# Optimization experiments

Hardware: AMD Instinct MI355X
Metric: run time of the kernel (lower is better)

The kernel has to match this reference:

```python
import jax, jax.numpy as jnp
import numpy as np

HID = 3584   # hidden_size
NH = 28      # num_attention_heads
NKV = 4      # num_key_value_heads
HD = 128     # head_dim
S = 4        # packed samples
L = 1024     # tokens per sample (sample_lens = [L]*S)
T = S * L
THETA = 1000000.0
EPS = 1e-6


def rmsnorm(x, w):
    # Qwen2NavitRMSNorm (fp32 math)
    v = jnp.mean(x * x, axis=-1, keepdims=True)
    return w * (x * jax.lax.rsqrt(v + EPS))


def rotate_half(x):
    d = x.shape[-1] // 2
    return jnp.concatenate([-x[..., d:], x[..., :d]], axis=-1)


def setup_inputs() -> dict:
    key = jax.random.key(0)
    ks = jax.random.split(key, 12)
    sc = 0.02
    x = jax.random.normal(ks[0], (T, HID), jnp.float32)
    # rotary embeddings: positions restart per packed sample
    pos = jnp.tile(jnp.arange(L, dtype=jnp.float32), S)
    inv = 1.0 / (THETA ** (jnp.arange(0, HD, 2, dtype=jnp.float32) / HD))
    fr = pos[:, None] * inv[None, :]
    emb = jnp.concatenate([fr, fr], axis=-1)  # [T, HD]
    und_idx = jnp.arange(0, T, 2, dtype=jnp.int32)  # interleaved und/gen tokens
    gen_idx = jnp.arange(1, T, 2, dtype=jnp.int32)
    n = lambda k, shp: jax.random.normal(k, shp, jnp.float32) * sc
    return dict(
        packed_sequence=x, cos=jnp.cos(emb), sin=jnp.sin(emb),
        wq=n(ks[1], (NH * HD, HID)), bq=jnp.zeros((NH * HD,), jnp.float32),
        wk=n(ks[2], (NKV * HD, HID)), bk=jnp.zeros((NKV * HD,), jnp.float32),
        wv=n(ks[3], (NKV * HD, HID)), bv=jnp.zeros((NKV * HD,), jnp.float32),
        wo=n(ks[4], (HID, NH * HD)),
        wqg=n(ks[5], (NH * HD, HID)), bqg=jnp.zeros((NH * HD,), jnp.float32),
        wkg=n(ks[6], (NKV * HD, HID)), bkg=jnp.zeros((NKV * HD,), jnp.float32),
        wvg=n(ks[7], (NKV * HD, HID)), bvg=jnp.zeros((NKV * HD,), jnp.float32),
        wog=n(ks[8], (HID, NH * HD)),
        qn=jnp.ones((HD,), jnp.float32), kn=jnp.ones((HD,), jnp.float32),
        qng=jnp.ones((HD,), jnp.float32), kng=jnp.ones((HD,), jnp.float32),
        und_idx=und_idx, gen_idx=gen_idx,
    )


def reference(packed_sequence, cos, sin, wq, bq, wk, bk, wv, bv, wo,
              wqg, bqg, wkg, bkg, wvg, bvg, wog, qn, kn, qng, kng,
              und_idx, gen_idx):
    x = packed_sequence
    xu = x[und_idx]
    xg = x[gen_idx]

    def dual_proj(wu, bu, wg, bg, dim):
        out = jnp.zeros((T, dim), x.dtype)
        out = out.at[und_idx].set(xu @ wu.T + bu)
        out = out.at[gen_idx].set(xg @ wg.T + bg)
        return out

    q = dual_proj(wq, bq, wqg, bqg, NH * HD).reshape(T, NH, HD)
    k = dual_proj(wk, bk, wkg, bkg, NKV * HD).reshape(T, NKV, HD)
    v = dual_proj(wv, bv, wvg, bvg, NKV * HD).reshape(T, NKV, HD)

    # per-modality qk RMSNorm
    q = jnp.zeros_like(q).at[und_idx].set(rmsnorm(q[und_idx], qn)).at[gen_idx].set(rmsnorm(q[gen_idx], qng))
    k = jnp.zeros_like(k).at[und_idx].set(rmsnorm(k[und_idx], kn)).at[gen_idx].set(rmsnorm(k[gen_idx], kng))

    # RoPE (unsqueeze_dim=1 -> broadcast over heads)
    c = cos[:, None, :]
    s = sin[:, None, :]
    q = q * c + rotate_half(q) * s
    k = k * c + rotate_half(k) * s

    # GQA expand kv heads (consecutive repeat matches repeat+reshape in torch)
    grp = NH // NKV
    k = jnp.repeat(k, grp, axis=1)  # [T, NH, HD]
    v = jnp.repeat(v, grp, axis=1)

    # packed -> per-sample causal attention (all sample_lens equal)
    qh = q.reshape(S, L, NH, HD)
    kh = k.reshape(S, L, NH, HD)
    vh = v.reshape(S, L, NH, HD)
    scores = jnp.einsum('slhd,smhd->shlm', qh, kh) / np.float32(np.sqrt(HD))
    causal = jnp.tril(jnp.ones((L, L), bool))
    scores = jnp.where(causal, scores, jnp.float32(-1e30))
    p = jax.nn.softmax(scores, axis=-1)
    attn = jnp.einsum('shlm,smhd->slhd', p, vh).reshape(T, NH * HD)

    out = jnp.zeros((T, HID), x.dtype)
    out = out.at[und_idx].set(attn[und_idx] @ wo.T)
    out = out.at[gen_idx].set(attn[gen_idx] @ wog.T)
    return out
```

## Files before the change

### kernel.cpp

```cpp
#include <hip/hip_runtime.h>
#include <hip/hip_bf16.h>

#define T_TOK 4096
#define HID   3584
#define NH    28
#define NKV   4
#define HD    128
#define SEG   4
#define LSEQ  1024
#define KDIM  3584
#define BKG   64
#define NCVT  128

typedef __attribute__((ext_vector_type(8))) short bf16x8;
typedef __attribute__((ext_vector_type(4))) float f32x4;

#define GLOAD16(g, l) __builtin_amdgcn_global_load_lds( \
    (const __attribute__((address_space(1))) void*)(g), \
    (__attribute__((address_space(3))) void*)(l), 16, 0, 0)

__device__ __forceinline__ unsigned short f2bf(float f) {
    unsigned u = __float_as_uint(f);
    return (unsigned short)((u + 0x7fffu + ((u >> 16) & 1u)) >> 16);
}
__device__ __forceinline__ float bf2f(unsigned short u) {
    return __uint_as_float(((unsigned)u) << 16);
}

__device__ __forceinline__ f32x4 mfma16(bf16x8 a, bf16x8 b, f32x4 c) {
    return __builtin_amdgcn_mfma_f32_16x16x32_bf16(a, b, c, 0, 0, 0);
}


__global__ void cvt4_f32_bf16(const float* __restrict__ s0, const float* __restrict__ s1,
                              const float* __restrict__ s2, const float* __restrict__ s3,
                              unsigned short* __restrict__ d0, unsigned short* __restrict__ d1,
                              unsigned short* __restrict__ d2, unsigned short* __restrict__ d3,
                              int n4) {
    const float* s; unsigned short* d;
    switch (blockIdx.y) {
        case 0: s = s0; d = d0; break;
        case 1: s = s1; d = d1; break;
        case 2: s = s2; d = d2; break;
        default: s = s3; d = d3; break;
    }
    int i = blockIdx.x * 256 + threadIdx.x;
    if (i >= n4) return;
    float4 v = reinterpret_cast<const float4*>(s)[i];
    ushort4 o;
    o.x = f2bf(v.x); o.y = f2bf(v.y); o.z = f2bf(v.z); o.w = f2bf(v.w);
    reinterpret_cast<ushort4*>(d)[i] = o;
}

__global__ void cvt_x_split(const float* __restrict__ x,
                            unsigned short* __restrict__ xu, unsigned short* __restrict__ xg) {
    int i = blockIdx.x * 256 + threadIdx.x;
    int t = i / (HID / 4);
    int c = i - t * (HID / 4);
    float4 v = reinterpret_cast<const float4*>(x)[i];
    ushort4 o;
    o.x = f2bf(v.x); o.y = f2bf(v.y); o.z = f2bf(v.z); o.w = f2bf(v.w);
    unsigned short* dst = ((t & 1) ? xg : xu) + (size_t)(t >> 1) * HID + c * 4;
    *reinterpret_cast<ushort4*>(dst) = o;
}

__device__ __forceinline__ void gemm256_core(const unsigned short* __restrict__ Aptr,
                                             const unsigned short* __restrict__ Bptr,
                                             unsigned short* ldsbase, f32x4 (&acc)[8][4],
                                             int kb, int kend) {
    const int tid = threadIdx.x;
    const int lane = tid & 63, w = tid >> 6;
    const int wr = w >> 2, wc = w & 3;
    const int lr = lane & 15, lkg = lane >> 4;
    char* const L = (char*)ldsbase;

    int src_off[4];
#pragma unroll
    for (int j = 0; j < 4; j++) {
        int r = j * 64 + (tid >> 3);
        int clog = (tid & 7) ^ ((tid >> 3) & 7);
        src_off[j] = r * KDIM + clog * 8;
    }
    const int aoff0 = (wr * 128 + lr) * 128 + ((lkg ^ (lr & 7)) << 4);
    const int boff0 = (wc * 64 + lr) * 128 + ((lkg ^ (lr & 7)) << 4) + 32768;

    bf16x8 a[4][2], b[4][2];
#pragma unroll
    for (int m = 0; m < 8; m++)
#pragma unroll
        for (int n = 0; n < 4; n++) acc[m][n] = (f32x4){0.f, 0.f, 0.f, 0.f};

#define STG_A(buf, k0, h) do { _Pragma("unroll") for (int jj = 0; jj < 2; jj++) { \
    int j = (h) * 2 + jj; \
    GLOAD16(Aptr + src_off[j] + (k0), L + (buf) * 65536 + j * 8192 + tid * 16); } } while (0)
#define STG_B(buf, k0, h) do { _Pragma("unroll") for (int jj = 0; jj < 2; jj++) { \
    int j = (h) * 2 + jj; \
    GLOAD16(Bptr + src_off[j] + (k0), L + (buf) * 65536 + 32768 + j * 8192 + tid * 16); } } while (0)
#define RD_A(buf, mh) do { _Pragma("unroll") for (int mm = 0; mm < 4; mm++) { \
    int ro = (buf) * 65536 + aoff0 + ((mh) * 4 + mm) * 2048; \
    a[mm][0] = *(const bf16x8*)(L + ro); \
    a[mm][1] = *(const bf16x8*)(L + (ro ^ 64)); } } while (0)
#define RD_B(buf, nh) do { _Pragma("unroll") for (int nn = 0; nn < 2; nn++) { \
    int ro = (buf) * 65536 + boff0 + ((nh) * 2 + nn) * 2048; \
    b[(nh) * 2 + nn][0] = *(const bf16x8*)(L + ro); \
    b[(nh) * 2 + nn][1] = *(const bf16x8*)(L + (ro ^ 64)); } } while (0)
#define MM(mh, nh) do { _Pragma("unroll") for (int mm = 0; mm < 4; mm++) \
    _Pragma("unroll") for (int nn = 0; nn < 2; nn++) \
    _Pragma("unroll") for (int ks = 0; ks < 2; ks++) \
        acc[(mh) * 4 + mm][(nh) * 2 + nn] = \
            mfma16(a[mm][ks], b[(nh) * 2 + nn][ks], acc[(mh) * 4 + mm][(nh) * 2 + nn]); } while (0)
#define BAR   asm volatile("s_barrier" ::: "memory")
#define LGKM0 do { asm volatile("s_waitcnt lgkmcnt(0)" ::: "memory"); \
                   __builtin_amdgcn_sched_barrier(0); } while (0)
#define VMC4  asm volatile("s_waitcnt vmcnt(4)" ::: "memory")
#define PHI   __builtin_amdgcn_s_setprio(1)
#define PLO   __builtin_amdgcn_s_setprio(0)

    STG_A(0, kb, 0); STG_A(0, kb, 1); STG_B(0, kb, 0); STG_B(0, kb, 1);
    STG_B(1, kb + BKG, 0); STG_B(1, kb + BKG, 1);
    VMC4;
    BAR;

    const int iters = (kend - kb) / (2 * BKG);
#pragma unroll 1
    for (int t = 0; t < iters; ++t) {
        int k1 = kb + (2 * t + 1) * BKG;
        int k2 = kb + (2 * t + 2) * BKG; if (k2 > kend - BKG) k2 = kend - BKG;
        int k3 = kb + (2 * t + 3) * BKG; if (k3 > kend - BKG) k3 = kend - BKG;
        RD_A(0, 0); RD_B(0, 0); STG_A(1, k1, 0);
        BAR; LGKM0; PHI; MM(0, 0); PLO; BAR;
        RD_B(0, 1); STG_A(1, k1, 1);
        BAR; LGKM0; PHI; MM(0, 1); PLO; BAR;
        RD_A(0, 1); STG_B(0, k2, 0);
        BAR; LGKM0; PHI; MM(1, 0); PLO; BAR;
        STG_B(0, k2, 1);
        BAR; LGKM0; PHI; MM(1, 1); PLO; VMC4; BAR;
        RD_A(1, 0); RD_B(1, 0); STG_A(0, k2, 0);
        BAR; LGKM0; PHI; MM(0, 0); PLO; BAR;
        RD_B(1, 1); STG_A(0, k2, 1);
        BAR; LGKM0; PHI; MM(0, 1); PLO; BAR;
        RD_A(1, 1); STG_B(1, k3, 0);
        BAR; LGKM0; PHI; MM(1, 0); PLO; BAR;
        STG_B(1, k3, 1);
        BAR; LGKM0; PHI; MM(1, 1); PLO; VMC4; BAR;
    }
    asm volatile("s_waitcnt vmcnt(0)" ::: "memory");

#undef STG_A
#undef STG_B
#undef RD_A
#undef RD_B
#undef MM
#undef BAR
#undef LGKM0
#undef VMC4
#undef PHI
#undef PLO
}

__global__ __launch_bounds__(512, 2) void qkv_gemm8(
    const unsigned short* __restrict__ xu, const unsigned short* __restrict__ xg,
    const unsigned short* __restrict__ wq0, const unsigned short* __restrict__ wk0,
    const unsigned short* __restrict__ wv0, const unsigned short* __restrict__ wq1,
    const unsigned short* __restrict__ wk1, const unsigned short* __restrict__ wv1,
    const float* __restrict__ bq0, const float* __restrict__ bk0, const float* __restrict__ bv0,
    const float* __restrict__ bq1, const float* __restrict__ bk1, const float* __restrict__ bv1,
    unsigned short* __restrict__ qp, unsigned short* __restrict__ kp,
    unsigned short* __restrict__ vp) {
    __shared__ unsigned short lds[65536];
    const int bid = blockIdx.x;
    int nb, ks, bm, kb, klen;
    if (bid < 448) {
        nb = bid >> 5;
        int rem = bid & 31;
        ks = rem >> 4; bm = rem & 15;
        kb = ks * 1792; klen = 1792;
    } else {
        int e = bid - 448;
        int g = e >> 6;
        int rem = e & 63;
        ks = rem >> 4; bm = rem & 15;
        nb = 14 + g;
        kb = ks * 896; klen = 896;
    }
    const int par = bm >> 3, mb = bm & 7;
    const unsigned short* A = (par ? xg : xu) + (size_t)mb * 256 * KDIM;
    const unsigned short* W;
    const float* bias;
    unsigned short* C;
    int ldc, col0;
    if (nb < 14) {
        W = (par ? wq1 : wq0) + (size_t)nb * 256 * KDIM;
        bias = (par ? bq1 : bq0); C = qp; ldc = NH * HD; col0 = nb * 256;
    } else if (nb < 16) {
        W = (par ? wk1 : wk0) + (size_t)(nb - 14) * 256 * KDIM;
        bias = (par ? bk1 : bk0); C = kp; ldc = NKV * HD; col0 = (nb - 14) * 256;
    } else {
        W = (par ? wv1 : wv0) + (size_t)(nb - 16) * 256 * KDIM;
        bias = (par ? bv1 : bv0); C = vp; ldc = NKV * HD; col0 = (nb - 16) * 256;
    }
    C += (size_t)ks * T_TOK * ldc;
    f32x4 acc[8][4];
    gemm256_core(A, W, lds, acc, kb, kb + klen);

    const int lane = threadIdx.x & 63, w = threadIdx.x >> 6;
    const int wr = w >> 2, wc = w & 3, lr = lane & 15, lkg = lane >> 4;
#pragma unroll
    for (int n = 0; n < 4; n++) {
        int colt = col0 + wc * 64 + n * 16 + lr;
        float bb = (ks == 0) ? bias[colt] : 0.f;
#pragma unroll
        for (int m = 0; m < 8; m++) {
#pragma unroll
            for (int rg = 0; rg < 4; rg++) {
                int tr = mb * 256 + wr * 128 + m * 16 + lkg * 4 + rg;
                int tok = 2 * tr + par;
                C[(size_t)tok * ldc + colt] = f2bf(acc[m][n][rg] + bb);
            }
        }
    }
}

__global__ __launch_bounds__(512, 2) void oproj_gemm8(
    const unsigned short* __restrict__ au, const unsigned short* __restrict__ ag,
    const unsigned short* __restrict__ wo0, const unsigned short* __restrict__ wo1,
    float* __restrict__ out) {
    __shared__ unsigned short lds[65536];
    const int bid = blockIdx.x;
    const int x = bid & 7, i = bid >> 3;
    const int nb = i >> 1, bm = x * 2 + (i & 1);
    const int par = bm >> 3, mb = bm & 7;
    const unsigned short* A = (par ? ag : au) + (size_t)mb * 256 * KDIM;
    const unsigned short* W = (par ? wo1 : wo0) + (size_t)nb * 256 * KDIM;
    f32x4 acc[8][4];
    gemm256_core(A, W, lds, acc, 0, KDIM);

    const int lane = threadIdx.x & 63, w = threadIdx.x >> 6;
    const int wr = w >> 2, wc = w & 3, lr = lane & 15, lkg = lane >> 4;
#pragma unroll
    for (int n = 0; n < 4; n++) {
        int col = nb * 256 + wc * 64 + n * 16 + lr;
#pragma unroll
        for (int m = 0; m < 8; m++) {
#pragma unroll
            for (int rg = 0; rg < 4; rg++) {
                int tr = mb * 256 + wr * 128 + m * 16 + lkg * 4 + rg;
                int tok = 2 * tr + par;
                out[(size_t)tok * HID + col] = acc[m][n][rg];
            }
        }
    }
}

__global__ void normrope2(const unsigned short* __restrict__ qp, const unsigned short* __restrict__ kp,
                          const unsigned short* __restrict__ vp,
                          const float* __restrict__ cosb, const float* __restrict__ sinb,
                          const float* __restrict__ qn, const float* __restrict__ kn,
                          const float* __restrict__ qng, const float* __restrict__ kng,
                          unsigned short* __restrict__ q_bf, unsigned short* __restrict__ k_bf,
                          unsigned short* __restrict__ vT) {
    if (blockIdx.y == 8) {
        if (blockIdx.x >= 1024) return;
        const int u = blockIdx.x * 2 + (threadIdx.x >> 7);
        const int d = threadIdx.x & 127;
        const int sh = u >> 7, lb = u & 127;
        const int s = sh >> 2, hv = sh & 3;
        const size_t S = (size_t)T_TOK * NKV * HD;
        unsigned short tmp[8];
#pragma unroll
        for (int i = 0; i < 8; i++) {
            size_t idx = ((size_t)(s * LSEQ + lb * 8 + i)) * (NKV * HD) + hv * HD + d;
            tmp[i] = f2bf(bf2f(vp[idx]) + bf2f(vp[S + idx]) +
                          bf2f(vp[2 * S + idx]) + bf2f(vp[3 * S + idx]));
        }
        *(bf16x8*)(vT + ((size_t)sh * HD + d) * LSEQ + lb * 8) = *(bf16x8*)tmp;
        return;
    }
    const int t = blockIdx.x, w = threadIdx.x >> 6, lane = threadIdx.x & 63;
    const int h = blockIdx.y * 4 + w;
    const bool isq = (h < 28);
    float v0, v1;
    if (isq) {
        const unsigned short* src = qp + (size_t)t * (NH * HD) + h * HD;
        const size_t S = (size_t)T_TOK * NH * HD;
        v0 = bf2f(src[lane]) + bf2f(src[S + lane]);
        v1 = bf2f(src[lane + 64]) + bf2f(src[S + lane + 64]);
    } else {
        const unsigned short* src = kp + (size_t)t * (NKV * HD) + (h - 28) * HD;
        const size_t S = (size_t)T_TOK * NKV * HD;
        v0 = bf2f(src[lane]) + bf2f(src[S + lane]) + bf2f(src[2 * S + lane]) + bf2f(src[3 * S + lane]);
        v1 = bf2f(src[lane + 64]) + bf2f(src[S + lane + 64]) +
             bf2f(src[2 * S + lane + 64]) + bf2f(src[3 * S + lane + 64]);
    }
    float ss = v0 * v0 + v1 * v1;
#pragma unroll
    for (int off = 32; off >= 1; off >>= 1) ss += __shfl_xor(ss, off, 64);
    float inv = rsqrtf(ss * (1.f / 128.f) + 1e-6f);
    const float* wn = isq ? ((t & 1) ? qng : qn) : ((t & 1) ? kng : kn);
    float n0 = v0 * inv * wn[lane], n1 = v1 * inv * wn[lane + 64];
    float c0 = cosb[(size_t)t * HD + lane], c1 = cosb[(size_t)t * HD + lane + 64];
    float s0 = sinb[(size_t)t * HD + lane], s1 = sinb[(size_t)t * HD + lane + 64];
    float o0 = n0 * c0 - n1 * s0;
    float o1 = n1 * c1 + n0 * s1;
    unsigned short* dst = isq ? q_bf + (size_t)t * (NH * HD) + h * HD
                              : k_bf + (size_t)t * (NKV * HD) + (h - 28) * HD;
    dst[lane] = f2bf(o0);
    dst[lane + 64] = f2bf(o1);
}

__global__ __launch_bounds__(512, 4) void attn_fwd(
    const unsigned short* __restrict__ q_bf, const unsigned short* __restrict__ k_bf,
    const unsigned short* __restrict__ vT,
    unsigned short* __restrict__ au, unsigned short* __restrict__ ag,
    const float* __restrict__ wof, const float* __restrict__ wogf,
    unsigned short* __restrict__ wob, unsigned short* __restrict__ wogb) {
    __shared__ unsigned short kt[2][64 * 128];
    __shared__ unsigned short vt[2][128 * 64];
    __shared__ unsigned short pt[8][16 * 64];

    const int bid = blockIdx.x;
    const int tid = threadIdx.x;
    if (bid < NCVT) {
        const size_t n4 = (size_t)KDIM * KDIM / 4;
        for (size_t i = (size_t)bid * 512 + tid; i < 2 * n4; i += (size_t)NCVT * 512) {
            const float* sp = (i < n4) ? wof : wogf;
            unsigned short* dp = (i < n4) ? wob : wogb;
            size_t j = (i < n4) ? i : i - n4;
            float4 v = reinterpret_cast<const float4*>(sp)[j];
            ushort4 o;
            o.x = f2bf(v.x); o.y = f2bf(v.y); o.z = f2bf(v.z); o.w = f2bf(v.w);
            reinterpret_cast<ushort4*>(dp)[j] = o;
        }
        return;
    }
    const int e = bid - NCVT;
    const int qbk = 7 - (e / 112);
    const int rem = e % 112;
    const int h = rem >> 2, s = rem & 3;
    const int hk = h / 7;
    const int lane = tid & 63, w = tid >> 6;
    const int lr = lane & 15, lkg = lane >> 4;
    const int qg = qbk * 128 + w * 16 + lr;

    bf16x8 qf[4];
    {
        const unsigned short* qp =
            q_bf + ((size_t)(s * LSEQ + qg)) * (NH * HD) + h * HD;
#pragma unroll
        for (int kk = 0; kk < 4; kk++) qf[kk] = *(const bf16x8*)(qp + kk * 32 + lkg * 8);
    }
    asm volatile("s_waitcnt vmcnt(0)" ::: "memory");

    float m_r = -1e30f, l_r = 0.f;
    f32x4 accO[8];
#pragma unroll
    for (int dn = 0; dn < 8; dn++) accO[dn] = (f32x4){0.f, 0.f, 0.f, 0.f};

    const float scale = 0.08838834764831843f;
    const int nkt = 2 * qbk + 2;

#define STAGE_KV(buf, ktile) do { _Pragma("unroll") for (int i = 0; i < 2; i++) { \
    int o = i * 8192 + tid * 16; \
    { int r = o >> 8; int sc = ((o >> 4) & 15) ^ (r & 7); \
      GLOAD16(k_bf + ((size_t)(s * LSEQ + (ktile) * 64 + r)) * (NKV * HD) + hk * HD + sc * 8, \
              (char*)kt[buf] + o); } \
    { int r = o >> 7; int sc = ((o >> 4) & 7) ^ (r & 7); \
      GLOAD16(vT + ((size_t)((s * NKV + hk) * HD + r)) * LSEQ + (ktile) * 64 + sc * 8, \
              (char*)vt[buf] + o); } } } while (0)

    STAGE_KV(0, 0);

#pragma unroll 1
    for (int ktile = 0; ktile < nkt; ++ktile) {
        const int cur = ktile & 1;
        if (ktile + 1 < nkt) {
            STAGE_KV(cur ^ 1, ktile + 1);
            asm volatile("s_waitcnt vmcnt(4)" ::: "memory");
        } else {
            asm volatile("s_waitcnt vmcnt(0)" ::: "memory");
        }
        asm volatile("s_barrier" ::: "memory");

        f32x4 accT[4];
#pragma unroll
        for (int n = 0; n < 4; n++) accT[n] = (f32x4){0.f, 0.f, 0.f, 0.f};
#pragma unroll
        for (int n = 0; n < 4; n++) {
            int r = n * 16 + lr;
#pragma unroll
            for (int kk = 0; kk < 4; kk++) {
                bf16x8 kf = *(const bf16x8*)((const char*)kt[cur] + r * 256 +
                                             (((kk * 4 + lkg) ^ (r & 7)) << 4));
                accT[n] = mfma16(kf, qf[kk], accT[n]);
            }
        }
        float mnew = -1e30f;
#pragma unroll
        for (int n = 0; n < 4; n++) {
#pragma unroll
            for (int rg = 0; rg < 4; rg++) {
                int kvg = ktile * 64 + n * 16 + lkg * 4 + rg;
                float sv = accT[n][rg] * scale;
                sv = (kvg <= qg) ? sv : -1e30f;
                accT[n][rg] = sv;
                mnew = fmaxf(mnew, sv);
            }
        }
        mnew = fmaxf(mnew, __shfl_xor(mnew, 16, 64));
        mnew = fmaxf(mnew, __shfl_xor(mnew, 32, 64));
        if (__any(mnew > m_r + 8.f)) {
            float mc = fmaxf(m_r, mnew);
            float alpha = __expf(m_r - mc);
            m_r = mc;
            l_r *= alpha;
            float ab[4];
#pragma unroll
            for (int rg = 0; rg < 4; rg++) ab[rg] = __shfl(alpha, lkg * 4 + rg, 64);
#pragma unroll
            for (int dn = 0; dn < 8; dn++)
#pragma unroll
                for (int rg = 0; rg < 4; rg++) accO[dn][rg] *= ab[rg];
        }
        float ls = 0.f;
#pragma unroll
        for (int n = 0; n < 4; n++) {
            unsigned short p4[4];
#pragma unroll
            for (int rg = 0; rg < 4; rg++) {
                float p = __expf(accT[n][rg] - m_r);
                ls += p;
                p4[rg] = f2bf(p);
            }
            int byte = lr * 128 + ((((n * 2 + (lkg >> 1)) ^ (lr & 7))) << 4) + (lkg & 1) * 8;
            *(uint2*)((char*)pt[w] + byte) = *(uint2*)p4;
        }
        ls += __shfl_xor(ls, 16, 64);
        ls += __shfl_xor(ls, 32, 64);
        l_r += ls;
#pragma unroll
        for (int kk2 = 0; kk2 < 2; kk2++) {
            bf16x8 pf = *(const bf16x8*)((const char*)pt[w] + lr * 128 +
                                         (((kk2 * 4 + lkg) ^ (lr & 7)) << 4));
#pragma unroll
            for (int dn = 0; dn < 8; dn++) {
                int r2 = dn * 16 + lr;
                bf16x8 vf = *(const bf16x8*)((const char*)vt[cur] + r2 * 128 +
                                             (((kk2 * 4 + lkg) ^ (r2 & 7)) << 4));
                accO[dn] = mfma16(pf, vf, accO[dn]);
            }
        }
        asm volatile("s_barrier" ::: "memory");
    }
#undef STAGE_KV

    float lb4[4];
#pragma unroll
    for (int rg = 0; rg < 4; rg++) lb4[rg] = __shfl(l_r, lkg * 4 + rg, 64);
#pragma unroll
    for (int dn = 0; dn < 8; dn++) {
#pragma unroll
        for (int rg = 0; rg < 4; rg++) {
            int row = qbk * 128 + w * 16 + lkg * 4 + rg;
            int t = s * LSEQ + row;
            unsigned short* dst = ((t & 1) ? ag : au) + (size_t)(t >> 1) * (NH * HD) +
                                  h * HD + dn * 16 + lr;
            *dst = f2bf(accO[dn][rg] / lb4[rg]);
        }
    }
}

extern "C" void kernel_launch(void* const* d_in, const int* in_sizes, int n_in,
                              void* d_out, int out_size, void* d_ws, size_t ws_size,
                              hipStream_t stream) {
    const float* x    = (const float*)d_in[0];
    const float* cosb = (const float*)d_in[1];
    const float* sinb = (const float*)d_in[2];
    const float* wq   = (const float*)d_in[3];
    const float* bq   = (const float*)d_in[4];
    const float* wk   = (const float*)d_in[5];
    const float* bk   = (const float*)d_in[6];
    const float* wv   = (const float*)d_in[7];
    const float* bv   = (const float*)d_in[8];
    const float* wo   = (const float*)d_in[9];
    const float* wqg  = (const float*)d_in[10];
    const float* bqg  = (const float*)d_in[11];
    const float* wkg  = (const float*)d_in[12];
    const float* bkg  = (const float*)d_in[13];
    const float* wvg  = (const float*)d_in[14];
    const float* bvg  = (const float*)d_in[15];
    const float* wog  = (const float*)d_in[16];
    const float* qn   = (const float*)d_in[17];
    const float* kn   = (const float*)d_in[18];
    const float* qng  = (const float*)d_in[19];
    const float* kng  = (const float*)d_in[20];
    float* out = (float*)d_out;

    char* ws = (char*)d_ws;
    size_t off = 0;
    auto alloc = [&](size_t bytes) -> char* {
        char* p = ws + off;
        off += (bytes + 255) & ~(size_t)255;
        return p;
    };
    const size_t WQ_E = (size_t)3584 * 3584;
    const size_t WK_E = (size_t)512 * 3584;
    unsigned short* wqb  = (unsigned short*)alloc(WQ_E * 2);
    unsigned short* wqgb = (unsigned short*)alloc(WQ_E * 2);
    unsigned short* wob  = (unsigned short*)alloc(WQ_E * 2);
    unsigned short* wogb = (unsigned short*)alloc(WQ_E * 2);
    unsigned short* wkb  = (unsigned short*)alloc(WK_E * 2);
    unsigned short* wkgb = (unsigned short*)alloc(WK_E * 2);
    unsigned short* wvb  = (unsigned short*)alloc(WK_E * 2);
    unsigned short* wvgb = (unsigned short*)alloc(WK_E * 2);
    unsigned short* xu   = (unsigned short*)alloc((size_t)2048 * HID * 2);
    unsigned short* xg   = (unsigned short*)alloc((size_t)2048 * HID * 2);
    unsigned short* qp = (unsigned short*)alloc((size_t)2 * T_TOK * (NH * HD) * 2);
    unsigned short* kp = (unsigned short*)alloc((size_t)4 * T_TOK * (NKV * HD) * 2);
    unsigned short* vp = (unsigned short*)alloc((size_t)4 * T_TOK * (NKV * HD) * 2);
    unsigned short* q_bf = wqb;
    unsigned short* k_bf = wqb + (size_t)T_TOK * (NH * HD);
    unsigned short* vTb  = k_bf + (size_t)T_TOK * (NKV * HD);
    unsigned short* au = qp;
    unsigned short* ag = au + (size_t)2048 * (NH * HD);

    if (ws_size < off) return;

    cvt_x_split<<<T_TOK * (HID / 4) / 256, 256, 0, stream>>>(x, xu, xg);
    cvt4_f32_bf16<<<dim3((int)(WQ_E / 4 / 256), 2), 256, 0, stream>>>(
        wq, wqg, wq, wqg, wqb, wqgb, wqb, wqgb, (int)(WQ_E / 4));
    cvt4_f32_bf16<<<dim3((int)(WK_E / 4 / 256), 4), 256, 0, stream>>>(
        wk, wkg, wv, wvg, wkb, wkgb, wvb, wvgb, (int)(WK_E / 4));

    qkv_gemm8<<<dim3(704), 512, 0, stream>>>(xu, xg, wqb, wkb, wvb, wqgb, wkgb, wvgb,
                                             bq, bk, bv, bqg, bkg, bvg, qp, kp, vp);
    normrope2<<<dim3(T_TOK, 9), 256, 0, stream>>>(qp, kp, vp, cosb, sinb,
                                                  qn, kn, qng, kng, q_bf, k_bf, vTb);
    attn_fwd<<<dim3(NCVT + 896), 512, 0, stream>>>(q_bf, k_bf, vTb, au, ag,
                                                   wo, wog, wob, wogb);
    oproj_gemm8<<<dim3(224), 512, 0, stream>>>(au, ag, wob, wogb, out);
}
```

Before: 408.4 us.

## Drop split-K for Q projection and fuse front conversion kernels

```diff
diff --git a/kernel.cpp b/kernel.cpp
--- a/kernel.cpp
+++ b/kernel.cpp
@@ -31,37 +31,46 @@
     return __builtin_amdgcn_mfma_f32_16x16x32_bf16(a, b, c, 0, 0, 0);
 }
 
-
-__global__ void cvt4_f32_bf16(const float* __restrict__ s0, const float* __restrict__ s1,
-                              const float* __restrict__ s2, const float* __restrict__ s3,
-                              unsigned short* __restrict__ d0, unsigned short* __restrict__ d1,
-                              unsigned short* __restrict__ d2, unsigned short* __restrict__ d3,
-                              int n4) {
+#define XN4  3670016
+#define WQ4  3211264
+#define WK4  458752
+__global__ void cvt_front(const float* __restrict__ x,
+                          const float* __restrict__ wq, const float* __restrict__ wqg,
+                          const float* __restrict__ wk, const float* __restrict__ wkg,
+                          const float* __restrict__ wv, const float* __restrict__ wvg,
+                          unsigned short* __restrict__ xu, unsigned short* __restrict__ xg,
+                          unsigned short* __restrict__ wqb, unsigned short* __restrict__ wqgb,
+                          unsigned short* __restrict__ wkb, unsigned short* __restrict__ wkgb,
+                          unsigned short* __restrict__ wvb, unsigned short* __restrict__ wvgb) {
+    size_t i = (size_t)blockIdx.x * 256 + threadIdx.x;
+    if (i < XN4) {
+        int t = (int)(i / (HID / 4));
+        int c = (int)(i - (size_t)t * (HID / 4));
+        float4 v = reinterpret_cast<const float4*>(x)[i];
+        ushort4 o;
+        o.x = f2bf(v.x); o.y = f2bf(v.y); o.z = f2bf(v.z); o.w = f2bf(v.w);
+        unsigned short* dst = ((t & 1) ? xg : xu) + (size_t)(t >> 1) * HID + c * 4;
+        *reinterpret_cast<ushort4*>(dst) = o;
+        return;
+    }
+    i -= XN4;
     const float* s; unsigned short* d;
-    switch (blockIdx.y) {
-        case 0: s = s0; d = d0; break;
-        case 1: s = s1; d = d1; break;
-        case 2: s = s2; d = d2; break;
-        default: s = s3; d = d3; break;
-    }
-    int i = blockIdx.x * 256 + threadIdx.x;
-    if (i >= n4) return;
+    if (i < 2 * (size_t)WQ4) {
+        if (i < WQ4) { s = wq; d = wqb; } else { i -= WQ4; s = wqg; d = wqgb; }
+    } else {
+        i -= 2 * (size_t)WQ4;
+        size_t seg = i / WK4; i -= seg * WK4;
+        switch (seg) {
+            case 0: s = wk;  d = wkb;  break;
+            case 1: s = wkg; d = wkgb; break;
+            case 2: s = wv;  d = wvb;  break;
+            default: s = wvg; d = wvgb; break;
+        }
+    }
     float4 v = reinterpret_cast<const float4*>(s)[i];
     ushort4 o;
     o.x = f2bf(v.x); o.y = f2bf(v.y); o.z = f2bf(v.z); o.w = f2bf(v.w);
     reinterpret_cast<ushort4*>(d)[i] = o;
-}
-
-__global__ void cvt_x_split(const float* __restrict__ x,
-                            unsigned short* __restrict__ xu, unsigned short* __restrict__ xg) {
-    int i = blockIdx.x * 256 + threadIdx.x;
-    int t = i / (HID / 4);
-    int c = i - t * (HID / 4);
-    float4 v = reinterpret_cast<const float4*>(x)[i];
-    ushort4 o;
-    o.x = f2bf(v.x); o.y = f2bf(v.y); o.z = f2bf(v.z); o.w = f2bf(v.w);
-    unsigned short* dst = ((t & 1) ? xg : xu) + (size_t)(t >> 1) * HID + c * 4;
-    *reinterpret_cast<ushort4*>(dst) = o;
 }
 
 __device__ __forceinline__ void gemm256_core(const unsigned short* __restrict__ Aptr,
@@ -170,18 +179,16 @@
     __shared__ unsigned short lds[65536];
     const int bid = blockIdx.x;
     int nb, ks, bm, kb, klen;
-    if (bid < 448) {
-        nb = bid >> 5;
-        int rem = bid & 31;
-        ks = rem >> 4; bm = rem & 15;
-        kb = ks * 1792; klen = 1792;
-    } else {
-        int e = bid - 448;
-        int g = e >> 6;
-        int rem = e & 63;
+    if (bid < 256) {
+        int g = bid >> 6;
+        int rem = bid & 63;
         ks = rem >> 4; bm = rem & 15;
         nb = 14 + g;
         kb = ks * 896; klen = 896;
+    } else {
+        int e = bid - 256;
+        nb = e >> 4; bm = e & 15;
+        ks = 0; kb = 0; klen = KDIM;
     }
     const int par = bm >> 3, mb = bm & 7;
     const unsigned short* A = (par ? xg : xu) + (size_t)mb * 256 * KDIM;
@@ -194,12 +201,13 @@
         bias = (par ? bq1 : bq0); C = qp; ldc = NH * HD; col0 = nb * 256;
     } else if (nb < 16) {
         W = (par ? wk1 : wk0) + (size_t)(nb - 14) * 256 * KDIM;
-        bias = (par ? bk1 : bk0); C = kp; ldc = NKV * HD; col0 = (nb - 14) * 256;
+        bias = (par ? bk1 : bk0); C = kp + (size_t)ks * T_TOK * (NKV * HD);
+        ldc = NKV * HD; col0 = (nb - 14) * 256;
     } else {
         W = (par ? wv1 : wv0) + (size_t)(nb - 16) * 256 * KDIM;
-        bias = (par ? bv1 : bv0); C = vp; ldc = NKV * HD; col0 = (nb - 16) * 256;
-    }
-    C += (size_t)ks * T_TOK * ldc;
+        bias = (par ? bv1 : bv0); C = vp + (size_t)ks * T_TOK * (NKV * HD);
+        ldc = NKV * HD; col0 = (nb - 16) * 256;
+    }
     f32x4 acc[8][4];
     gemm256_core(A, W, lds, acc, kb, kb + klen);
 
@@ -282,9 +290,8 @@
     float v0, v1;
     if (isq) {
         const unsigned short* src = qp + (size_t)t * (NH * HD) + h * HD;
-        const size_t S = (size_t)T_TOK * NH * HD;
-        v0 = bf2f(src[lane]) + bf2f(src[S + lane]);
-        v1 = bf2f(src[lane + 64]) + bf2f(src[S + lane + 64]);
+        v0 = bf2f(src[lane]);
+        v1 = bf2f(src[lane + 64]);
     } else {
         const unsigned short* src = kp + (size_t)t * (NKV * HD) + (h - 28) * HD;
         const size_t S = (size_t)T_TOK * NKV * HD;
@@ -514,7 +521,7 @@
     unsigned short* wvgb = (unsigned short*)alloc(WK_E * 2);
     unsigned short* xu   = (unsigned short*)alloc((size_t)2048 * HID * 2);
     unsigned short* xg   = (unsigned short*)alloc((size_t)2048 * HID * 2);
-    unsigned short* qp = (unsigned short*)alloc((size_t)2 * T_TOK * (NH * HD) * 2);
+    unsigned short* qp = (unsigned short*)alloc((size_t)T_TOK * (NH * HD) * 2);
     unsigned short* kp = (unsigned short*)alloc((size_t)4 * T_TOK * (NKV * HD) * 2);
     unsigned short* vp = (unsigned short*)alloc((size_t)4 * T_TOK * (NKV * HD) * 2);
     unsigned short* q_bf = wqb;
@@ -525,13 +532,11 @@
 
     if (ws_size < off) return;
 
-    cvt_x_split<<<T_TOK * (HID / 4) / 256, 256, 0, stream>>>(x, xu, xg);
-    cvt4_f32_bf16<<<dim3((int)(WQ_E / 4 / 256), 2), 256, 0, stream>>>(
-        wq, wqg, wq, wqg, wqb, wqgb, wqb, wqgb, (int)(WQ_E / 4));
-    cvt4_f32_bf16<<<dim3((int)(WK_E / 4 / 256), 4), 256, 0, stream>>>(
-        wk, wkg, wv, wvg, wkb, wkgb, wvb, wvgb, (int)(WK_E / 4));
-
-    qkv_gemm8<<<dim3(704), 512, 0, stream>>>(xu, xg, wqb, wkb, wvb, wqgb, wkgb, wvgb,
+    cvt_front<<<dim3((XN4 + 2 * WQ4 + 4 * WK4) / 256), 256, 0, stream>>>(
+        x, wq, wqg, wk, wkg, wv, wvg,
+        xu, xg, wqb, wqgb, wkb, wkgb, wvb, wvgb);
+
+    qkv_gemm8<<<dim3(480), 512, 0, stream>>>(xu, xg, wqb, wkb, wvb, wqgb, wkgb, wvgb,
                                              bq, bk, bv, bqg, bkg, bvg, qp, kp, vp);
     normrope2<<<dim3(T_TOK, 9), 256, 0, stream>>>(qp, kp, vp, cosb, sinb,
                                                   qn, kn, qng, kng, q_bf, k_bf, vTb);
```

After: 394.0 us. -3.5%, faster.
